# Kernel tuning notes

Hardware: AMD Instinct MI355X
Metric: run time of the kernel (lower is better)

The kernel has to match this reference:

```python
import jax, jax.numpy as jnp
import numpy as np

D_MODEL = 1024
N_HEADS = 16
HEAD_DIM = D_MODEL // N_HEADS
D_FF = 4 * D_MODEL
EPS = 1e-5


def _layer_norm(h, g, b):
    m = jnp.mean(h, axis=-1, keepdims=True)
    v = jnp.mean(jnp.square(h - m), axis=-1, keepdims=True)
    return (h - m) * jax.lax.rsqrt(v + EPS) * g + b


def setup_inputs() -> dict:
    key = jax.random.key(0)
    ks = jax.random.split(key, 10)
    B, S, D = 4, 2048, D_MODEL
    scale = 0.02
    inp = {
        "x": jax.random.normal(ks[0], (B, S, D), dtype=jnp.float32),
        "Wq": scale * jax.random.normal(ks[1], (D, D), dtype=jnp.float32),
        "Wk": scale * jax.random.normal(ks[2], (D, D), dtype=jnp.float32),
        "Wv": scale * jax.random.normal(ks[3], (D, D), dtype=jnp.float32),
        "Wo": scale * jax.random.normal(ks[4], (D, D), dtype=jnp.float32),
        "ln1_g": jnp.ones((D,), dtype=jnp.float32),
        "ln1_b": jnp.zeros((D,), dtype=jnp.float32),
        "ln2_g": jnp.ones((D,), dtype=jnp.float32),
        "ln2_b": jnp.zeros((D,), dtype=jnp.float32),
        "W1": scale * jax.random.normal(ks[5], (D, D_FF), dtype=jnp.float32),
        "b1": jnp.zeros((D_FF,), dtype=jnp.float32),
        "W2": scale * jax.random.normal(ks[6], (D_FF, D), dtype=jnp.float32),
        "b2": jnp.zeros((D,), dtype=jnp.float32),
        "Wc": scale * jax.random.normal(ks[7], (D, 1), dtype=jnp.float32),
        "bc": jnp.zeros((1,), dtype=jnp.float32),
    }
    return inp


def reference(x, Wq, Wk, Wv, Wo, ln1_g, ln1_b, ln2_g, ln2_b, W1, b1, W2, b2, Wc, bc):
    B, S, D = x.shape
    H, hd = N_HEADS, HEAD_DIM
    # --- causal self-attention (pre-LN) ---
    h = _layer_norm(x, ln1_g, ln1_b)
    q = (h @ Wq).reshape(B, S, H, hd).transpose(0, 2, 1, 3)  # [B,H,S,hd]
    k = (h @ Wk).reshape(B, S, H, hd).transpose(0, 2, 1, 3)
    v = (h @ Wv).reshape(B, S, H, hd).transpose(0, 2, 1, 3)
    scores = jnp.einsum("bhqd,bhkd->bhqk", q, k) / jnp.sqrt(jnp.asarray(hd, x.dtype))
    causal = jnp.triu(jnp.ones((S, S), dtype=bool), k=1)
    scores = jnp.where(causal[None, None, :, :], -jnp.inf, scores)
    attn = jax.nn.softmax(scores, axis=-1)
    ctx = jnp.einsum("bhqk,bhkd->bhqd", attn, v).transpose(0, 2, 1, 3).reshape(B, S, D)
    x1 = x + ctx @ Wo
    # --- FFN (pre-LN, ReLU) ---
    h2 = _layer_norm(x1, ln2_g, ln2_b)
    ff = jax.nn.relu(h2 @ W1 + b1) @ W2 + b2
    x_out = x1 + ff
    # --- adaptive confidence gate: mean-pool seq -> Linear -> sigmoid -> batch mean ---
    pooled = jnp.mean(x_out, axis=1)  # [B,D]
    conf = jnp.mean(jax.nn.sigmoid(pooled @ Wc + bc), axis=0)  # [1]
    return x_out, conf
```

## Files before the change

kernel.cpp:

```cpp
#include <hip/hip_runtime.h>
#include <hip/hip_bf16.h>

typedef __hip_bfloat16 bf16;
typedef __attribute__((ext_vector_type(8))) short short8;
typedef __attribute__((ext_vector_type(4))) float f32x4;

#define D_MODELC 1024
#define D_FFC    4096
#define NHEADS   16
#define HDIM     64
#define SEQLEN   2048
#define BATCHN   4
#define MTOT     (BATCHN * SEQLEN)

__device__ __forceinline__ void async16(void* lds, const void* g) {
  __builtin_amdgcn_global_load_lds(
      (const __attribute__((address_space(1))) unsigned int*)g,
      (__attribute__((address_space(3))) unsigned int*)lds, 16, 0, 0);
}

__global__ __launch_bounds__(256) void transpose_bf16_k(
    const float* __restrict__ src, bf16* __restrict__ dst, int R, int C, float scale) {
  __shared__ float tile[32][33];
  int tx = threadIdx.x & 31, ty = threadIdx.x >> 5;
  int r0 = blockIdx.y * 32, c0 = blockIdx.x * 32;
#pragma unroll
  for (int i = 0; i < 4; i++) {
    int r = ty + i * 8;
    tile[r][tx] = src[(size_t)(r0 + r) * C + c0 + tx];
  }
  __syncthreads();
#pragma unroll
  for (int i = 0; i < 4; i++) {
    int c = ty + i * 8;
    dst[(size_t)(c0 + c) * R + r0 + tx] = __float2bfloat16(tile[tx][c] * scale);
  }
}

__global__ __launch_bounds__(256) void ln_bf16_k(
    const float* __restrict__ x, const float* __restrict__ g,
    const float* __restrict__ b, bf16* __restrict__ out) {
  int row = blockIdx.x;
  int t = threadIdx.x;
  f32x4 v = ((const f32x4*)(x + (size_t)row * D_MODELC))[t];
  float s = v[0] + v[1] + v[2] + v[3];
  float ss = v[0] * v[0] + v[1] * v[1] + v[2] * v[2] + v[3] * v[3];
#pragma unroll
  for (int m = 1; m < 64; m <<= 1) {
    s += __shfl_xor(s, m);
    ss += __shfl_xor(ss, m);
  }
  __shared__ float red[8];
  int w = t >> 6, l = t & 63;
  if (l == 0) { red[w] = s; red[4 + w] = ss; }
  __syncthreads();
  s = red[0] + red[1] + red[2] + red[3];
  ss = red[4] + red[5] + red[6] + red[7];
  float mean = s * (1.0f / D_MODELC);
  float var = ss * (1.0f / D_MODELC) - mean * mean;
  float rs = rsqrtf(var + 1e-5f);
  f32x4 gv = ((const f32x4*)g)[t];
  f32x4 bv = ((const f32x4*)b)[t];
  unsigned short u[4];
#pragma unroll
  for (int j = 0; j < 4; j++) {
    float o = (v[j] - mean) * rs * gv[j] + bv[j];
    u[j] = __bfloat16_as_ushort(__float2bfloat16(o));
  }
  unsigned int lo = (unsigned int)u[0] | ((unsigned int)u[1] << 16);
  unsigned int hi = (unsigned int)u[2] | ((unsigned int)u[3] << 16);
  ((uint2*)(out + (size_t)row * D_MODELC))[t] = make_uint2(lo, hi);
}

#define BM 128
#define BN 128
#define BKK 64

enum { EPI_QKV = 0, EPI_RESID = 1, EPI_BIAS_RELU = 2, EPI_BIAS_RESID = 3 };

template <int EPI>
__global__ __launch_bounds__(256) void gemm_nt(
    const bf16* __restrict__ A, const bf16* __restrict__ BT, int M, int N, int K,
    const float* __restrict__ bias, const float* __restrict__ resid,
    float* __restrict__ outF, bf16* __restrict__ outB) {
  __shared__ bf16 As[BM * BKK];
  __shared__ bf16 Bs[BN * BKK];
  const int t = threadIdx.x;
  const int l = t & 63;
  const int w = t >> 6;
  const int wm = w >> 1, wn = w & 1;

  int nwg = gridDim.x * gridDim.y;
  int bid = blockIdx.y * gridDim.x + blockIdx.x;
  if ((nwg & 7) == 0) {
    int q8 = nwg >> 3;
    bid = (bid & 7) * q8 + (bid >> 3);
  }
  const int bx = bid % gridDim.x, by = bid / gridDim.x;
  const int m0 = by * BM, n0 = bx * BN;
  const int lr = l & 15, lkg = l >> 4;

  f32x4 acc[4][4];
#pragma unroll
  for (int i = 0; i < 4; i++)
#pragma unroll
    for (int j = 0; j < 4; j++) acc[i][j] = (f32x4){0.f, 0.f, 0.f, 0.f};

  const char* Abase = (const char*)(A + (size_t)m0 * K);
  const char* Bbase = (const char*)(BT + (size_t)n0 * K);

  for (int k0 = 0; k0 < K; k0 += BKK) {
#pragma unroll
    for (int c = 0; c < 4; c++) {
      int off = (c * 256 + t) * 16;
      int r = off >> 7;
      int sg = ((off >> 4) & 7) ^ (r & 7);
      async16((char*)As + off, Abase + ((size_t)r * K + k0) * 2 + sg * 16);
      async16((char*)Bs + off, Bbase + ((size_t)r * K + k0) * 2 + sg * 16);
    }
    __syncthreads();
    short8 a[2][4], b[2][4];
#pragma unroll
    for (int kk = 0; kk < 2; kk++) {
#pragma unroll
      for (int mi = 0; mi < 4; mi++) {
        int row = wm * 64 + mi * 16 + lr;
        int sl = (kk * 4 + lkg) ^ (row & 7);
        a[kk][mi] = *(const short8*)((const char*)As + row * 128 + sl * 16);
      }
#pragma unroll
      for (int ni = 0; ni < 4; ni++) {
        int row = wn * 64 + ni * 16 + lr;
        int sl = (kk * 4 + lkg) ^ (row & 7);
        b[kk][ni] = *(const short8*)((const char*)Bs + row * 128 + sl * 16);
      }
    }
#pragma unroll
    for (int kk = 0; kk < 2; kk++)
#pragma unroll
      for (int mi = 0; mi < 4; mi++)
#pragma unroll
        for (int ni = 0; ni < 4; ni++)
          acc[mi][ni] = __builtin_amdgcn_mfma_f32_16x16x32_bf16(a[kk][mi], b[kk][ni], acc[mi][ni], 0, 0, 0);
    __syncthreads();
  }

#pragma unroll
  for (int mi = 0; mi < 4; mi++) {
#pragma unroll
    for (int ni = 0; ni < 4; ni++) {
#pragma unroll
      for (int j = 0; j < 4; j++) {
        int gm = m0 + wm * 64 + mi * 16 + ((l >> 4) * 4) + j;
        int gn = n0 + wn * 64 + ni * 16 + lr;
        float v = acc[mi][ni][j];
        if constexpr (EPI == EPI_QKV) {
          int sel = gn >> 10, d = gn & 1023;
          int b_ = gm >> 11, s_ = gm & 2047;
          int h2 = d >> 6, dd = d & 63;
          size_t bh = (size_t)b_ * NHEADS + h2;
          size_t dst;
          if (sel < 2) {
            dst = (size_t)sel * ((size_t)MTOT * D_MODELC) +
                  (bh * SEQLEN + s_) * HDIM + dd;
          } else {
            dst = 2 * ((size_t)MTOT * D_MODELC) +
                  (bh * HDIM + dd) * SEQLEN + s_;
          }
          outB[dst] = __float2bfloat16(v);
        } else if constexpr (EPI == EPI_RESID) {
          size_t idx = (size_t)gm * N + gn;
          outF[idx] = resid[idx] + v;
        } else if constexpr (EPI == EPI_BIAS_RELU) {
          float z = v + bias[gn];
          outB[(size_t)gm * N + gn] = __float2bfloat16(z > 0.f ? z : 0.f);
        } else {
          size_t idx = (size_t)gm * N + gn;
          outF[idx] = resid[idx] + v + bias[gn];
        }
      }
    }
  }
}

#define KVB 64
#define PSTR 76

__global__ __launch_bounds__(256) void attn_k(
    const bf16* __restrict__ qg, const bf16* __restrict__ kg,
    const bf16* __restrict__ vtg, bf16* __restrict__ ctx) {
  const int bid = blockIdx.x;
  const int qt = (SEQLEN / KVB - 1) - (bid >> 6);
  const int bh = bid & 63;
  const int q0 = qt * 64;
  const int t = threadIdx.x, w = t >> 6, l = t & 63;
  const int lr = l & 15, lkg = l >> 4, lk = lkg * 8;

  const bf16* Q  = qg  + (size_t)bh * SEQLEN * HDIM;
  const bf16* Kg = kg  + (size_t)bh * SEQLEN * HDIM;
  const bf16* Vt = vtg + (size_t)bh * HDIM * SEQLEN;

  __shared__ bf16 Ks[KVB * PSTR];
  __shared__ bf16 Vs[HDIM * PSTR];
  __shared__ bf16 Ps[4][16 * PSTR];

  short8 qf[2];
  const int qrow = q0 + w * 16 + lr;
#pragma unroll
  for (int kk = 0; kk < 2; kk++)
    qf[kk] = *(const short8*)&Q[(size_t)qrow * HDIM + kk * 32 + lk];

  const short8 bones = {0x3F80, 0x3F80, 0x3F80, 0x3F80, 0x3F80, 0x3F80, 0x3F80, 0x3F80};

  f32x4 o[4];
  f32x4 ol = (f32x4){0.f, 0.f, 0.f, 0.f};
#pragma unroll
  for (int nh = 0; nh < 4; nh++) o[nh] = (f32x4){0.f, 0.f, 0.f, 0.f};

  const int srow = t >> 3;
  const int scc  = (t & 7) * 8;

  const int ntiles = qt + 1;
  for (int tkv = 0; tkv < ntiles; tkv++) {
    const int kv0 = tkv * KVB;
#pragma unroll
    for (int r = 0; r < 2; r++) {
      int row = srow + r * 32;
      short8 kv = *(const short8*)&Kg[(size_t)(kv0 + row) * HDIM + scc];
      *(short8*)&Ks[row * PSTR + scc] = kv;
      short8 vv = *(const short8*)&Vt[(size_t)row * SEQLEN + kv0 + scc];
      *(short8*)&Vs[row * PSTR + scc] = vv;
    }
    __syncthreads();

    short8 kf[4][2];
#pragma unroll
    for (int ni = 0; ni < 4; ni++)
#pragma unroll
      for (int kk = 0; kk < 2; kk++)
        kf[ni][kk] = *(const short8*)&Ks[(ni * 16 + lr) * PSTR + kk * 32 + lk];
    f32x4 s[4];
#pragma unroll
    for (int ni = 0; ni < 4; ni++) {
      f32x4 a = (f32x4){0.f, 0.f, 0.f, 0.f};
#pragma unroll
      for (int kk = 0; kk < 2; kk++)
        a = __builtin_amdgcn_mfma_f32_16x16x32_bf16(qf[kk], kf[ni][kk], a, 0, 0, 0);
      s[ni] = a;
    }
    if (tkv == ntiles - 1) {
#pragma unroll
      for (int ni = 0; ni < 4; ni++)
#pragma unroll
        for (int j = 0; j < 4; j++) {
          int qq = q0 + w * 16 + lkg * 4 + j;
          int kv = kv0 + ni * 16 + lr;
          if (kv > qq) s[ni][j] = -1e30f;
        }
    }
#pragma unroll
    for (int ni = 0; ni < 4; ni++)
#pragma unroll
      for (int j = 0; j < 4; j++)
        ((short*)Ps[w])[(lkg * 4 + j) * PSTR + ni * 16 + lr] =
            (short)__bfloat16_as_ushort(__float2bfloat16(exp2f(s[ni][j])));
#pragma unroll
    for (int kk = 0; kk < 2; kk++) {
      short8 pa = *(const short8*)&Ps[w][lr * PSTR + kk * 32 + lk];
      ol = __builtin_amdgcn_mfma_f32_16x16x32_bf16(pa, bones, ol, 0, 0, 0);
#pragma unroll
      for (int nh = 0; nh < 4; nh++) {
        short8 vb = *(const short8*)&Vs[(nh * 16 + lr) * PSTR + kk * 32 + lk];
        o[nh] = __builtin_amdgcn_mfma_f32_16x16x32_bf16(pa, vb, o[nh], 0, 0, 0);
      }
    }
    __syncthreads();
  }

  const int b_ = bh >> 4, h_ = bh & 15;
#pragma unroll
  for (int j = 0; j < 4; j++) {
    float inv = 1.0f / ol[j];
    int qq = q0 + w * 16 + lkg * 4 + j;
    size_t base = (((size_t)b_ * SEQLEN + qq) * NHEADS + h_) * HDIM;
#pragma unroll
    for (int nh = 0; nh < 4; nh++)
      ctx[base + nh * 16 + lr] = __float2bfloat16(o[nh][j] * inv);
  }
}

__global__ __launch_bounds__(256) void pool_partial_k(
    const float* __restrict__ xo, float* __restrict__ part) {
  int blk = blockIdx.x;
  int b_ = blk >> 4, ch = blk & 15;
  int t = threadIdx.x;
  f32x4 acc = (f32x4){0.f, 0.f, 0.f, 0.f};
  const float* base = xo + ((size_t)b_ * SEQLEN + (size_t)ch * 128) * D_MODELC;
  for (int r = 0; r < 128; r++)
    acc += ((const f32x4*)(base + (size_t)r * D_MODELC))[t];
  ((f32x4*)(part + (size_t)blk * D_MODELC))[t] = acc;
}

__global__ __launch_bounds__(256) void conf_k(
    const float* __restrict__ part, const float* __restrict__ Wc,
    const float* __restrict__ bc, float* __restrict__ outc) {
  int t = threadIdx.x;
  __shared__ float red[4];
  float total = 0.f;
  for (int b_ = 0; b_ < BATCHN; b_++) {
    f32x4 sum = (f32x4){0.f, 0.f, 0.f, 0.f};
    for (int ch = 0; ch < 16; ch++)
      sum += ((const f32x4*)(part + (size_t)(b_ * 16 + ch) * D_MODELC))[t];
    f32x4 wv = ((const f32x4*)Wc)[t];
    float d = (sum[0] * wv[0] + sum[1] * wv[1] + sum[2] * wv[2] + sum[3] * wv[3]) * (1.0f / SEQLEN);
#pragma unroll
    for (int m = 1; m < 64; m <<= 1) d += __shfl_xor(d, m);
    int wq = t >> 6, l = t & 63;
    if (l == 0) red[wq] = d;
    __syncthreads();
    float z = red[0] + red[1] + red[2] + red[3] + bc[0];
    total += 1.0f / (1.0f + __expf(-z));
    __syncthreads();
  }
  if (t == 0) outc[0] = total * (1.0f / BATCHN);
}

extern "C" void kernel_launch(void* const* d_in, const int* in_sizes, int n_in,
                              void* d_out, int out_size, void* d_ws, size_t ws_size,
                              hipStream_t stream) {
  const float* x    = (const float*)d_in[0];
  const float* Wq   = (const float*)d_in[1];
  const float* Wk   = (const float*)d_in[2];
  const float* Wv   = (const float*)d_in[3];
  const float* Wo   = (const float*)d_in[4];
  const float* ln1g = (const float*)d_in[5];
  const float* ln1b = (const float*)d_in[6];
  const float* ln2g = (const float*)d_in[7];
  const float* ln2b = (const float*)d_in[8];
  const float* W1   = (const float*)d_in[9];
  const float* b1   = (const float*)d_in[10];
  const float* W2   = (const float*)d_in[11];
  const float* b2   = (const float*)d_in[12];
  const float* Wc   = (const float*)d_in[13];
  const float* bc   = (const float*)d_in[14];

  char* ws = (char*)d_ws;
  const size_t MB = 1024 * 1024;
  bf16* qkv   = (bf16*)(ws);
  bf16* ctx   = (bf16*)(ws + 48 * MB);
  bf16* ff1   = (bf16*)(ws);
  bf16* h     = (bf16*)(ws + 64 * MB);
  bf16* WqkvT = (bf16*)(ws + 80 * MB);
  bf16* WoT   = (bf16*)(ws + 86 * MB);
  bf16* W1T   = (bf16*)(ws + 88 * MB);
  bf16* W2T   = (bf16*)(ws + 96 * MB);
  float* part = (float*)(ws + 104 * MB);

  float* xout = (float*)d_out;
  dim3 blk(256);

  const float SCL2 = 0.125f * 1.44269504f;

  transpose_bf16_k<<<dim3(32, 32), blk, 0, stream>>>(Wq, WqkvT, 1024, 1024, SCL2);
  transpose_bf16_k<<<dim3(32, 32), blk, 0, stream>>>(Wk, WqkvT + 1024 * 1024, 1024, 1024, 1.0f);
  transpose_bf16_k<<<dim3(32, 32), blk, 0, stream>>>(Wv, WqkvT + 2 * 1024 * 1024, 1024, 1024, 1.0f);
  transpose_bf16_k<<<dim3(32, 32), blk, 0, stream>>>(Wo, WoT, 1024, 1024, 1.0f);
  transpose_bf16_k<<<dim3(128, 32), blk, 0, stream>>>(W1, W1T, 1024, 4096, 1.0f);
  transpose_bf16_k<<<dim3(32, 128), blk, 0, stream>>>(W2, W2T, 4096, 1024, 1.0f);

  ln_bf16_k<<<MTOT, blk, 0, stream>>>(x, ln1g, ln1b, h);
  gemm_nt<EPI_QKV><<<dim3(3072 / BN, MTOT / BM), blk, 0, stream>>>(
      h, WqkvT, MTOT, 3072, 1024, nullptr, nullptr, nullptr, qkv);
  attn_k<<<dim3((SEQLEN / KVB) * 64), blk, 0, stream>>>(
      qkv, qkv + (size_t)MTOT * D_MODELC, qkv + 2 * (size_t)MTOT * D_MODELC, ctx);
  gemm_nt<EPI_RESID><<<dim3(1024 / BN, MTOT / BM), blk, 0, stream>>>(
      ctx, WoT, MTOT, 1024, 1024, nullptr, x, xout, nullptr);
  ln_bf16_k<<<MTOT, blk, 0, stream>>>(xout, ln2g, ln2b, h);
  gemm_nt<EPI_BIAS_RELU><<<dim3(4096 / BN, MTOT / BM), blk, 0, stream>>>(
      h, W1T, MTOT, 4096, 1024, b1, nullptr, nullptr, ff1);
  gemm_nt<EPI_BIAS_RESID><<<dim3(1024 / BN, MTOT / BM), blk, 0, stream>>>(
      ff1, W2T, MTOT, 1024, 4096, b2, xout, xout, nullptr);
  pool_partial_k<<<64, blk, 0, stream>>>(xout, part);
  conf_k<<<1, blk, 0, stream>>>(part, Wc, bc, xout + (size_t)MTOT * D_MODELC);
}
```

Baseline: 427.5 us.

## Switch GEMMs to 256x256 tiles with 512 threads and double-buffered LDS

Replaces the 128x128 single-buffered GEMM with a 256x256 tile kernel run by 8 waves. Each wave computes a 128x64 sub-tile. The next K slice is prefetched asynchronously into a second LDS buffer while the current one is consumed. The goal is more data reuse per global load and latency hidden behind MFMA work. In exchange, LDS use grows to about 128KB per block, which limits occupancy to one block per CU. The N=1024 GEMMs now launch only 128 workgroups, which can leave many CUs idle.

```diff
diff --git a/kernel.cpp b/kernel.cpp
--- a/kernel.cpp
+++ b/kernel.cpp
@@ -72,87 +72,92 @@
   ((uint2*)(out + (size_t)row * D_MODELC))[t] = make_uint2(lo, hi);
 }
 
-#define BM 128
-#define BN 128
-#define BKK 64
+#define GBM 256
+#define GBN 256
+#define GBK 64
 
 enum { EPI_QKV = 0, EPI_RESID = 1, EPI_BIAS_RELU = 2, EPI_BIAS_RESID = 3 };
 
 template <int EPI>
-__global__ __launch_bounds__(256) void gemm_nt(
-    const bf16* __restrict__ A, const bf16* __restrict__ BT, int M, int N, int K,
+__global__ __launch_bounds__(512) void gemm256(
+    const bf16* __restrict__ A, const bf16* __restrict__ BT, int N, int K,
     const float* __restrict__ bias, const float* __restrict__ resid,
     float* __restrict__ outF, bf16* __restrict__ outB) {
-  __shared__ bf16 As[BM * BKK];
-  __shared__ bf16 Bs[BN * BKK];
+  __shared__ bf16 As[2][GBM * GBK];
+  __shared__ bf16 Bs[2][GBN * GBK];
   const int t = threadIdx.x;
-  const int l = t & 63;
-  const int w = t >> 6;
-  const int wm = w >> 1, wn = w & 1;
-
-  int nwg = gridDim.x * gridDim.y;
-  int bid = blockIdx.y * gridDim.x + blockIdx.x;
-  if ((nwg & 7) == 0) {
-    int q8 = nwg >> 3;
-    bid = (bid & 7) * q8 + (bid >> 3);
-  }
-  const int bx = bid % gridDim.x, by = bid / gridDim.x;
-  const int m0 = by * BM, n0 = bx * BN;
+  const int l = t & 63, wid = t >> 6;
+  const int wr = wid >> 2, wc = wid & 3;
   const int lr = l & 15, lkg = l >> 4;
 
-  f32x4 acc[4][4];
-#pragma unroll
-  for (int i = 0; i < 4; i++)
+  int nwg = gridDim.x;
+  int bid = blockIdx.x;
+  int sb = (bid & 7) * (nwg >> 3) + (bid >> 3);
+  const int by = sb & 31;
+  const int bx = sb >> 5;
+  const int m0 = by * GBM, n0 = bx * GBN;
+
+  f32x4 acc[8][4];
+#pragma unroll
+  for (int i = 0; i < 8; i++)
 #pragma unroll
     for (int j = 0; j < 4; j++) acc[i][j] = (f32x4){0.f, 0.f, 0.f, 0.f};
 
   const char* Abase = (const char*)(A + (size_t)m0 * K);
   const char* Bbase = (const char*)(BT + (size_t)n0 * K);
 
-  for (int k0 = 0; k0 < K; k0 += BKK) {
-#pragma unroll
-    for (int c = 0; c < 4; c++) {
-      int off = (c * 256 + t) * 16;
-      int r = off >> 7;
-      int sg = ((off >> 4) & 7) ^ (r & 7);
-      async16((char*)As + off, Abase + ((size_t)r * K + k0) * 2 + sg * 16);
-      async16((char*)Bs + off, Bbase + ((size_t)r * K + k0) * 2 + sg * 16);
-    }
-    __syncthreads();
-    short8 a[2][4], b[2][4];
+#define STAGE256(buf, k0)                                                        \
+  {                                                                              \
+    _Pragma("unroll")                                                            \
+    for (int c = 0; c < 4; c++) {                                                \
+      int off = (c * 512 + t) * 16;                                              \
+      int rrow = off >> 7;                                                       \
+      int sg = ((off >> 4) & 7) ^ (rrow & 7);                                    \
+      async16((char*)As[buf] + off, Abase + ((size_t)rrow * K + (k0)) * 2 + sg * 16); \
+      async16((char*)Bs[buf] + off, Bbase + ((size_t)rrow * K + (k0)) * 2 + sg * 16); \
+    }                                                                            \
+  }
+
+  STAGE256(0, 0);
+  __syncthreads();
+  int cur = 0;
+  for (int k0 = 0; k0 < K; k0 += GBK) {
+    if (k0 + GBK < K) STAGE256(cur ^ 1, k0 + GBK);
+    const char* Ab = (const char*)As[cur];
+    const char* Bb = (const char*)Bs[cur];
 #pragma unroll
     for (int kk = 0; kk < 2; kk++) {
-#pragma unroll
-      for (int mi = 0; mi < 4; mi++) {
-        int row = wm * 64 + mi * 16 + lr;
+      short8 a[8], b[4];
+#pragma unroll
+      for (int mi = 0; mi < 8; mi++) {
+        int row = wr * 128 + mi * 16 + lr;
         int sl = (kk * 4 + lkg) ^ (row & 7);
-        a[kk][mi] = *(const short8*)((const char*)As + row * 128 + sl * 16);
+        a[mi] = *(const short8*)(Ab + row * 128 + sl * 16);
       }
 #pragma unroll
       for (int ni = 0; ni < 4; ni++) {
-        int row = wn * 64 + ni * 16 + lr;
+        int row = wc * 64 + ni * 16 + lr;
         int sl = (kk * 4 + lkg) ^ (row & 7);
-        b[kk][ni] = *(const short8*)((const char*)Bs + row * 128 + sl * 16);
+        b[ni] = *(const short8*)(Bb + row * 128 + sl * 16);
       }
-    }
-#pragma unroll
-    for (int kk = 0; kk < 2; kk++)
-#pragma unroll
-      for (int mi = 0; mi < 4; mi++)
+#pragma unroll
+      for (int mi = 0; mi < 8; mi++)
 #pragma unroll
         for (int ni = 0; ni < 4; ni++)
-          acc[mi][ni] = __builtin_amdgcn_mfma_f32_16x16x32_bf16(a[kk][mi], b[kk][ni], acc[mi][ni], 0, 0, 0);
-    __syncthreads();
-  }
-
-#pragma unroll
-  for (int mi = 0; mi < 4; mi++) {
+          acc[mi][ni] = __builtin_amdgcn_mfma_f32_16x16x32_bf16(a[mi], b[ni], acc[mi][ni], 0, 0, 0);
+    }
+    __syncthreads();
+    cur ^= 1;
+  }
+
+#pragma unroll
+  for (int mi = 0; mi < 8; mi++) {
 #pragma unroll
     for (int ni = 0; ni < 4; ni++) {
 #pragma unroll
       for (int j = 0; j < 4; j++) {
-        int gm = m0 + wm * 64 + mi * 16 + ((l >> 4) * 4) + j;
-        int gn = n0 + wn * 64 + ni * 16 + lr;
+        int gm = m0 + wr * 128 + mi * 16 + lkg * 4 + j;
+        int gn = n0 + wc * 64 + ni * 16 + lr;
         float v = acc[mi][ni][j];
         if constexpr (EPI == EPI_QKV) {
           int sel = gn >> 10, d = gn & 1023;
@@ -181,6 +186,7 @@
       }
     }
   }
+#undef STAGE256
 }
 
 #define KVB 64
@@ -358,6 +364,7 @@
 
   float* xout = (float*)d_out;
   dim3 blk(256);
+  dim3 blk512(512);
 
   const float SCL2 = 0.125f * 1.44269504f;
 
@@ -369,17 +376,17 @@
   transpose_bf16_k<<<dim3(32, 128), blk, 0, stream>>>(W2, W2T, 4096, 1024, 1.0f);
 
   ln_bf16_k<<<MTOT, blk, 0, stream>>>(x, ln1g, ln1b, h);
-  gemm_nt<EPI_QKV><<<dim3(3072 / BN, MTOT / BM), blk, 0, stream>>>(
-      h, WqkvT, MTOT, 3072, 1024, nullptr, nullptr, nullptr, qkv);
+  gemm256<EPI_QKV><<<dim3((3072 / GBN) * 32), blk512, 0, stream>>>(
+      h, WqkvT, 3072, 1024, nullptr, nullptr, nullptr, qkv);
   attn_k<<<dim3((SEQLEN / KVB) * 64), blk, 0, stream>>>(
       qkv, qkv + (size_t)MTOT * D_MODELC, qkv + 2 * (size_t)MTOT * D_MODELC, ctx);
-  gemm_nt<EPI_RESID><<<dim3(1024 / BN, MTOT / BM), blk, 0, stream>>>(
-      ctx, WoT, MTOT, 1024, 1024, nullptr, x, xout, nullptr);
+  gemm256<EPI_RESID><<<dim3((1024 / GBN) * 32), blk512, 0, stream>>>(
+      ctx, WoT, 1024, 1024, nullptr, x, xout, nullptr);
   ln_bf16_k<<<MTOT, blk, 0, stream>>>(xout, ln2g, ln2b, h);
-  gemm_nt<EPI_BIAS_RELU><<<dim3(4096 / BN, MTOT / BM), blk, 0, stream>>>(
-      h, W1T, MTOT, 4096, 1024, b1, nullptr, nullptr, ff1);
-  gemm_nt<EPI_BIAS_RESID><<<dim3(1024 / BN, MTOT / BM), blk, 0, stream>>>(
-      ff1, W2T, MTOT, 1024, 4096, b2, xout, xout, nullptr);
+  gemm256<EPI_BIAS_RELU><<<dim3((4096 / GBN) * 32), blk512, 0, stream>>>(
+      h, W1T, 4096, 1024, b1, nullptr, nullptr, ff1);
+  gemm256<EPI_BIAS_RESID><<<dim3((1024 / GBN) * 32), blk512, 0, stream>>>(
+      ff1, W2T, 1024, 4096, b2, xout, xout, nullptr);
   pool_partial_k<<<64, blk, 0, stream>>>(xout, part);
   conf_k<<<1, blk, 0, stream>>>(part, Wc, bc, xout + (size_t)MTOT * D_MODELC);
 }
```

Measured after the change: 503.9 us. 1.18x slower.
